# Kernel optimization log

Hardware: AMD Instinct MI355X
Metric: run time of the kernel (lower is better)

The kernel has to match this reference:

```python
import jax, jax.numpy as jnp
import numpy as np

B, H, K, T, OUT, NH = 512, 512, 6, 60, 2, 8

def _gelu(x):
    return jax.nn.gelu(x, approximate=False)  # torch nn.GELU default = exact erf

def _layernorm(x, g, b, eps=1e-5):
    m = jnp.mean(x, axis=-1, keepdims=True)
    v = jnp.var(x, axis=-1, keepdims=True)
    return (x - m) * jax.lax.rsqrt(v + eps) * g + b

def setup_inputs() -> dict:
    key = jax.random.key(0)
    ks = iter(jax.random.split(key, 40))
    def p(shape, scale=0.02):
        return jax.random.normal(next(ks), shape, dtype=jnp.float32) * scale
    return dict(
        interaction_ctx=p((B, H), 1.0),
        cooperative_ctx=p((B, H), 1.0),
        map_ctx=p((B, H), 1.0),
        mode_queries=p((K, H)),
        # context_proj: Linear(3H,H) -> GELU -> Linear(H,H)
        Wc1=p((3 * H, H)), bc1=jnp.zeros((H,), jnp.float32),
        Wc2=p((H, H)), bc2=jnp.zeros((H,), jnp.float32),
        # coarse_heads stacked over modes: Linear(H,2H)->GELU->Linear(2H,T*OUT)
        Wk1=p((K, H, 2 * H)), bk1=jnp.zeros((K, 2 * H), jnp.float32),
        Wk2=p((K, 2 * H, T * OUT)), bk2=jnp.zeros((K, T * OUT), jnp.float32),
        # traj_encoder: Linear(OUT,H)->GELU
        Wt=p((OUT, H)), bt=jnp.zeros((H,), jnp.float32),
        # refine_attn (MultiheadAttention) projections
        Wq_a=p((H, H)), bq_a=jnp.zeros((H,), jnp.float32),
        Wk_a=p((H, H)), bk_a=jnp.zeros((H,), jnp.float32),
        Wv_a=p((H, H)), bv_a=jnp.zeros((H,), jnp.float32),
        Wo_a=p((H, H)), bo_a=jnp.zeros((H,), jnp.float32),
        ln_g=jnp.ones((H,), jnp.float32), ln_b=jnp.zeros((H,), jnp.float32),
        # refine_heads stacked over modes: Linear(H,H)->GELU->Linear(H,OUT)
        Wr1=p((K, H, H)), br1=jnp.zeros((K, H), jnp.float32),
        Wr2=p((K, H, OUT)), br2=jnp.zeros((K, OUT), jnp.float32),
        # conf_head: Linear(H,64)->ReLU->Linear(64,1)
        Wf1=p((H, 64)), bf1=jnp.zeros((64,), jnp.float32),
        Wf2=p((64, 1)), bf2=jnp.zeros((1,), jnp.float32),
    )

def reference(interaction_ctx, cooperative_ctx, map_ctx, mode_queries,
              Wc1, bc1, Wc2, bc2, Wk1, bk1, Wk2, bk2, Wt, bt,
              Wq_a, bq_a, Wk_a, bk_a, Wv_a, bv_a, Wo_a, bo_a,
              ln_g, ln_b, Wr1, br1, Wr2, br2, Wf1, bf1, Wf2, bf2):
    # dropout layers are identity in eval mode
    combined = jnp.concatenate([interaction_ctx, cooperative_ctx, map_ctx], axis=-1)  # (B,3H)
    context = _gelu(combined @ Wc1 + bc1) @ Wc2 + bc2                                 # (B,H)
    mode_features = mode_queries[None, :, :] + context[:, None, :]                    # (B,K,H)

    # coarse heads: per-mode loop -> grouped GEMM over mode axis
    h = _gelu(jnp.einsum('bkh,khf->bkf', mode_features, Wk1) + bk1)                   # (B,K,2H)
    coarse = (jnp.einsum('bkf,kfo->bko', h, Wk2) + bk2).reshape(B, K, T, OUT)          # (B,K,T,OUT)

    traj_feats = _gelu(coarse @ Wt + bt)                                              # (B,K,T,H)

    # refine_attn: keys/values are context broadcast over T (all identical), so
    # softmax weights are exactly uniform and attention output == out_proj(v_ctx).
    # (grads through Wq_a/Wk_a are exactly zero for the same reason.)
    v = context @ Wv_a + bv_a                                                         # (B,H)
    attn_out = v @ Wo_a + bo_a                                                        # (B,H)

    refined_feats = _layernorm(traj_feats + attn_out[:, None, None, :], ln_g, ln_b)   # (B,K,T,H)

    # refine heads: grouped GEMM over mode axis
    r = _gelu(jnp.einsum('bkth,khf->bktf', refined_feats, Wr1) + br1[:, None, :])     # (B,K,T,H)
    offsets = jnp.einsum('bktf,kfo->bkto', r, Wr2) + br2[:, None, :]                  # (B,K,T,OUT)
    predictions = coarse + offsets

    conf = jax.nn.relu(mode_features @ Wf1 + bf1) @ Wf2 + bf2                         # (B,K,1)
    mode_probs = jax.nn.softmax(conf[..., 0], axis=-1)                                # (B,K)
    return predictions, mode_probs
```

## Files before the change

kernel.cpp:

```cpp
#include <hip/hip_runtime.h>
#include <math.h>

#define BB 512
#define HH 512
#define KK 6
#define TT 60
#define OO 2
#define H2 1024
#define TO 120
#define RFP 520
#define HSP 1032

typedef __bf16 bf16x8 __attribute__((ext_vector_type(8)));
typedef float  f32x4  __attribute__((ext_vector_type(4)));
typedef float  f32x16 __attribute__((ext_vector_type(16)));

__device__ __forceinline__ float bf2f(unsigned short u) {
    union { unsigned int i; float f; } v; v.i = ((unsigned int)u) << 16; return v.f;
}
__device__ __forceinline__ unsigned short f2bf(float f) {
    union { float f; unsigned int i; } v; v.f = f;
    unsigned int b = v.i;
    return (unsigned short)((b + 0x7FFFu + ((b >> 16) & 1u)) >> 16);
}
__device__ __forceinline__ unsigned int pack2bf(float a, float b) {
    union { __bf16 h[2]; unsigned int u; } v;
    v.h[0] = (__bf16)a; v.h[1] = (__bf16)b;
    return v.u;
}
__device__ __forceinline__ float gelu_exact(float x) {
    return 0.5f * x * (1.0f + erff(x * 0.70710678118654752f));
}

#if defined(__has_builtin)
#  if __has_builtin(__builtin_amdgcn_rcpf)
#    define FAST_RCP(x) __builtin_amdgcn_rcpf(x)
#  endif
#  if __has_builtin(__builtin_amdgcn_exp2f)
#    define FAST_EXP2(x) __builtin_amdgcn_exp2f(x)
#  endif
#endif
#ifndef FAST_RCP
#  define FAST_RCP(x) (1.0f / (x))
#endif
#ifndef FAST_EXP2
#  define FAST_EXP2(x) __expf((x) * 0.69314718056f)
#endif

__device__ __forceinline__ float gelu_cheap(float x) {
    float x2 = x * x;
    float z = x * fmaf(0.10294324f, x2, 2.3022082f);
    float e = FAST_EXP2(-z);
    return x * FAST_RCP(1.0f + e);
}

struct F8 { float v[8]; };
__device__ __forceinline__ F8 load8f(const float* p) {
    F8 r;
    float4 a = *(const float4*)p;
    float4 b = *(const float4*)(p + 4);
    r.v[0] = a.x; r.v[1] = a.y; r.v[2] = a.z; r.v[3] = a.w;
    r.v[4] = b.x; r.v[5] = b.y; r.v[6] = b.z; r.v[7] = b.w;
    return r;
}
__device__ __forceinline__ F8 load8b(const unsigned short* p) {
    ushort4 a = *(const ushort4*)p;
    ushort4 b = *(const ushort4*)(p + 4);
    F8 r;
    r.v[0] = bf2f(a.x); r.v[1] = bf2f(a.y); r.v[2] = bf2f(a.z); r.v[3] = bf2f(a.w);
    r.v[4] = bf2f(b.x); r.v[5] = bf2f(b.y); r.v[6] = bf2f(b.z); r.v[7] = bf2f(b.w);
    return r;
}

struct PKD { const float* src; unsigned short* dst; int F, N, NC, nch, steps, Z; };
struct PK8 { PKD e[8]; };

__global__ void k_pack(PK8 d) {
    int rid = blockIdx.x * 4 + (threadIdx.x >> 6);
    const int ln = threadIdx.x & 63;
    int i = 0;
    while (i < 7) {
        int tot = d.e[i].Z * d.e[i].nch * d.e[i].steps;
        if (rid < tot) break;
        rid -= tot; ++i;
    }
    const PKD e = d.e[i];
    const int per = e.nch * e.steps;
    const int z = rid / per;
    const int r = rid - z * per;
    const int nch = r / e.steps, step = r - nch * e.steps;
    const float* src = e.src + (size_t)z * e.F * e.N;
    unsigned short* dst = e.dst + ((size_t)z * per + r) * 512 + ln * 8;
    int f_base, n;
    if (e.NC == 16) { f_base = step * 32 + (ln >> 4) * 8; n = nch * 16 + (ln & 15); }
    else            { f_base = step * 16 + (ln >> 5) * 8; n = nch * 32 + (ln & 31); }
    if (n >= e.N) n = e.N - 1;
    unsigned int pk[4];
#pragma unroll
    for (int j = 0; j < 4; ++j) {
        unsigned short lo = f2bf(src[(size_t)(f_base + 2 * j) * e.N + n]);
        unsigned short hi = f2bf(src[(size_t)(f_base + 2 * j + 1) * e.N + n]);
        pk[j] = (unsigned int)lo | ((unsigned int)hi << 16);
    }
    *(uint4*)dst = make_uint4(pk[0], pk[1], pk[2], pk[3]);
}

template <bool CONCAT, bool GELU>
__launch_bounds__(256)
__global__ void k_gemm_m(const void* __restrict__ A0, const void* __restrict__ A1,
                         const void* __restrict__ A2, const unsigned short* __restrict__ BP,
                         const float* __restrict__ bias, unsigned short* __restrict__ C,
                         int Kd) {
    __shared__ __align__(16) unsigned short As[32 * RFP];
    const int tid = threadIdx.x;
    const int bm = blockIdx.x * 32;
    const int bn = blockIdx.y * 32;
    const int w = tid >> 6, ln = tid & 63;
    const int lane15 = ln & 15, quad = ln >> 4;
    const int mh = w >> 1;
    const int ng = w & 1;
    const int n = bn + ng * 16 + lane15;
    const int nchunks = Kd / HH;
    const int stepsTot = Kd / 32;
    const int nchB = blockIdx.y * 2 + ng;

    f32x4 acc0 = {0.f, 0.f, 0.f, 0.f};

    for (int kc = 0; kc < nchunks; ++kc) {
        {
            int r = tid >> 3, c0 = (tid & 7) * 64;
            unsigned short* dp = As + r * RFP + c0;
            if (CONCAT) {
                const float* src = (kc == 0) ? (const float*)A0
                                 : (kc == 1) ? (const float*)A1 : (const float*)A2;
                const float* sp = src + (bm + r) * HH + c0;
                for (int c = 0; c < 64; c += 8) {
                    F8 v = load8f(sp + c);
                    unsigned int pk[4];
#pragma unroll
                    for (int j = 0; j < 4; ++j)
                        pk[j] = pack2bf(v.v[2 * j], v.v[2 * j + 1]);
                    *(uint4*)(dp + c) = make_uint4(pk[0], pk[1], pk[2], pk[3]);
                }
            } else {
                const unsigned short* sp = (const unsigned short*)A0 + (bm + r) * HH + c0;
                for (int c = 0; c < 64; c += 8)
                    *(uint4*)(dp + c) = *(const uint4*)(sp + c);
            }
        }
        __syncthreads();
        const unsigned short* bp = BP + ((size_t)nchB * stepsTot + kc * 16) * 512 + ln * 8;
#pragma unroll
        for (int f0 = 0; f0 < HH; f0 += 32) {
            bf16x8 a0 = *(const bf16x8*)(As + (mh * 16 + lane15) * RFP + f0 + quad * 8);
            bf16x8 bf = *(const bf16x8*)(bp);
            bp += 512;
            acc0 = __builtin_amdgcn_mfma_f32_16x16x32_bf16(a0, bf, acc0, 0, 0, 0);
        }
        __syncthreads();
    }
    const float bb = bias[n];
#pragma unroll
    for (int reg = 0; reg < 4; ++reg) {
        float v0 = acc0[reg] + bb;
        if (GELU) v0 = gelu_exact(v0);
        C[(bm + mh * 16 + quad * 4 + reg) * HH + n] = f2bf(v0);
    }
}

__launch_bounds__(512)
__global__ void k_bcg(const unsigned short* __restrict__ ctx, const float* __restrict__ mq,
                      const unsigned short* __restrict__ Wk1P, const float* __restrict__ bk1,
                      const unsigned short* __restrict__ Wk2P, const float* __restrict__ bk2,
                      const unsigned short* __restrict__ Wf1P, const float* __restrict__ bf1,
                      const float* __restrict__ Wf2, const float* __restrict__ bf2v,
                      unsigned short* __restrict__ coarse_out, float* __restrict__ conf_out,
                      const unsigned short* __restrict__ WvP, const float* __restrict__ bv,
                      unsigned short* __restrict__ vout)
{
    __shared__ __align__(16) unsigned short shbuf[24832];

    const int tid = threadIdx.x;
    const int w = tid >> 6;
    const int ln = tid & 63;
    const int lane15 = ln & 15;
    const int quad = ln >> 4;

    if (blockIdx.x >= 192) {
        unsigned short* As = shbuf;
        const int gbid = blockIdx.x - 192;
        const int bm = (gbid & 15) * 32;
        const int gy = gbid >> 4;
        const int bn = gy * 64;
        const int mh = w >> 2;
        const int ng = w & 3;
        const int n = bn + ng * 16 + lane15;
        const int nchB = gy * 4 + ng;

        {
            int r = tid >> 4, c0 = (tid & 15) * 32;
            const unsigned short* sp = ctx + (bm + r) * HH + c0;
            unsigned short* dp = As + r * RFP + c0;
            for (int c = 0; c < 32; c += 8)
                *(uint4*)(dp + c) = *(const uint4*)(sp + c);
        }
        __syncthreads();
        f32x4 acc0 = {0.f, 0.f, 0.f, 0.f};
        const unsigned short* bp = WvP + (size_t)nchB * 16 * 512 + ln * 8;
#pragma unroll
        for (int f0 = 0; f0 < HH; f0 += 32) {
            bf16x8 a0 = *(const bf16x8*)(As + (mh * 16 + lane15) * RFP + f0 + quad * 8);
            bf16x8 bf = *(const bf16x8*)(bp);
            bp += 512;
            acc0 = __builtin_amdgcn_mfma_f32_16x16x32_bf16(a0, bf, acc0, 0, 0, 0);
        }
        const float bb = bv[n];
#pragma unroll
        for (int reg = 0; reg < 4; ++reg)
            vout[(bm + mh * 16 + quad * 4 + reg) * HH + n] = f2bf(acc0[reg] + bb);
        return;
    }

    unsigned short* mf = shbuf;
    unsigned short* hs = shbuf + 16 * RFP;
    const int k = blockIdx.x % KK;
    const int b0 = (blockIdx.x / KK) * 16;

    {
        int r = tid >> 5;
        int c0 = (tid & 31) * 16;
        const unsigned short* cp = ctx + (b0 + r) * HH + c0;
        const float* qp = mq + k * HH + c0;
        unsigned short* dp = mf + r * RFP + c0;
        for (int c = 0; c < 16; c += 8) {
            F8 cv = load8b(cp + c);
            F8 qv = load8f(qp + c);
            unsigned int pk[4];
#pragma unroll
            for (int j = 0; j < 4; ++j)
                pk[j] = pack2bf(cv.v[2 * j] + qv.v[2 * j], cv.v[2 * j + 1] + qv.v[2 * j + 1]);
            *(uint4*)(dp + c) = make_uint4(pk[0], pk[1], pk[2], pk[3]);
        }
    }
    __syncthreads();

    {
        const unsigned short* wk1p = Wk1P + (size_t)k * (64 * 16 * 512);
        const float* bk1p = bk1 + k * H2;
        for (int g = 0; g < 8; ++g) {
            const int n = w * 128 + g * 16 + lane15;
            f32x4 acc0 = {0.f,0.f,0.f,0.f};
            const unsigned short* bp = wk1p + (size_t)((w * 8 + g) * 16) * 512 + ln * 8;
#pragma unroll
            for (int f0 = 0; f0 < HH; f0 += 32) {
                bf16x8 a0 = *(const bf16x8*)(mf + lane15 * RFP + f0 + quad * 8);
                bf16x8 bf = *(const bf16x8*)(bp);
                bp += 512;
                acc0 = __builtin_amdgcn_mfma_f32_16x16x32_bf16(a0, bf, acc0, 0, 0, 0);
            }
            const float bias = bk1p[n];
#pragma unroll
            for (int reg = 0; reg < 4; ++reg)
                hs[(quad * 4 + reg) * HSP + n] = f2bf(gelu_exact(acc0[reg] + bias));
        }
    }
    __syncthreads();

    {
        const unsigned short* wk2p = Wk2P + (size_t)k * (8 * 32 * 512);
        const int n = w * 16 + lane15;
        f32x4 acc0 = {0.f,0.f,0.f,0.f};
        const unsigned short* bp = wk2p + (size_t)(w * 32) * 512 + ln * 8;
#pragma unroll
        for (int f0 = 0; f0 < H2; f0 += 32) {
            bf16x8 a0 = *(const bf16x8*)(hs + lane15 * HSP + f0 + quad * 8);
            bf16x8 bf = *(const bf16x8*)(bp);
            bp += 512;
            acc0 = __builtin_amdgcn_mfma_f32_16x16x32_bf16(a0, bf, acc0, 0, 0, 0);
        }
        if (n < TO) {
            const float bias = bk2[k * TO + n];
#pragma unroll
            for (int reg = 0; reg < 4; ++reg)
                coarse_out[((b0 + quad * 4 + reg) * KK + k) * TO + n] = f2bf(acc0[reg] + bias);
        }
    }

    if (w == 0) {
        f32x4 acc[4];
#pragma unroll
        for (int nt = 0; nt < 4; ++nt) { f32x4 z = {0.f,0.f,0.f,0.f}; acc[nt] = z; }
#pragma unroll
        for (int f0 = 0; f0 < HH; f0 += 32) {
            const int step = f0 >> 5;
            bf16x8 a0 = *(const bf16x8*)(mf + lane15 * RFP + f0 + quad * 8);
#pragma unroll
            for (int nt = 0; nt < 4; ++nt) {
                bf16x8 bf = *(const bf16x8*)(Wf1P + (size_t)(nt * 16 + step) * 512 + ln * 8);
                acc[nt] = __builtin_amdgcn_mfma_f32_16x16x32_bf16(a0, bf, acc[nt], 0, 0, 0);
            }
        }
        const float b2 = bf2v[0];
#pragma unroll
        for (int reg = 0; reg < 4; ++reg) {
            float s = 0.f;
#pragma unroll
            for (int nt = 0; nt < 4; ++nt) {
                const int n = nt * 16 + lane15;
                s = fmaf(fmaxf(acc[nt][reg] + bf1[n], 0.f), Wf2[n], s);
            }
#pragma unroll
            for (int off = 1; off < 16; off <<= 1) s += __shfl_xor(s, off);
            if (lane15 == 0)
                conf_out[(b0 + quad * 4 + reg) * KK + k] = s + b2;
        }
    }
}

__launch_bounds__(512, 4)
__global__ void k_ef(
    const unsigned short* __restrict__ attn, const unsigned short* __restrict__ coarse_ws,
    const float* __restrict__ Wt,  const float* __restrict__ bt,
    const float* __restrict__ lng, const float* __restrict__ lnb,
    const unsigned short* __restrict__ Wr1P, const float* __restrict__ br1,
    const float* __restrict__ Wr2, const float* __restrict__ br2,
    float* __restrict__ pred_out,
    const float* __restrict__ conf, float* __restrict__ probs)
{
    __shared__ __align__(16) unsigned short rf[64 * RFP];
    __shared__ float coarse[TO];
    __shared__ float br1s[HH];
    __shared__ float2 wr2s[HH];
    __shared__ float po2[8][64][2];

    const int tid = threadIdx.x;
    const int b = blockIdx.x / KK;
    const int k = blockIdx.x % KK;
    const int w = tid >> 6;
    const int ln = tid & 63;
    const int lane31 = ln & 31;
    const int hf = ln >> 5;
    const int cbase = ln * 8;

    const unsigned short* attb = attn + b * HH;

    if (tid < TO) coarse[tid] = bf2f(coarse_ws[(b * KK + k) * TO + tid]);
    br1s[tid] = br1[k * HH + tid];
    wr2s[tid] = ((const float2*)Wr2)[(size_t)k * HH + tid];

    if (k == 0 && tid == 448) {
        float v[KK]; float m = -1e30f;
#pragma unroll
        for (int i = 0; i < KK; ++i) { v[i] = conf[b * KK + i]; m = fmaxf(m, v[i]); }
        float s = 0.f;
#pragma unroll
        for (int i = 0; i < KK; ++i) { v[i] = __expf(v[i] - m); s += v[i]; }
        float inv = 1.0f / s;
#pragma unroll
        for (int i = 0; i < KK; ++i) probs[b * KK + i] = v[i] * inv;
    }
    __syncthreads();

    {
        F8 w0 = load8f(Wt + cbase);
        F8 w1 = load8f(Wt + HH + cbase);
        F8 b8 = load8f(bt + cbase);
        F8 g8 = load8f(lng + cbase);
        F8 bb8 = load8f(lnb + cbase);
        F8 a8 = load8b(attb + cbase);
#pragma unroll
        for (int g = 0; g < 2; ++g) {
            float x[4][8];
            float s[4], s2[4];
#pragma unroll
            for (int r = 0; r < 4; ++r) {
                const int t = w + 8 * (g * 4 + r);
                float ss = 0.f, ss2 = 0.f;
                if (t < 60) {
                    const float co0 = coarse[2 * t], co1 = coarse[2 * t + 1];
#pragma unroll
                    for (int j = 0; j < 8; ++j) {
                        float vv = fmaf(co0, w0.v[j], fmaf(co1, w1.v[j], b8.v[j]));
                        vv = gelu_cheap(vv) + a8.v[j];
                        x[r][j] = vv; ss += vv; ss2 = fmaf(vv, vv, ss2);
                    }
                } else {
#pragma unroll
                    for (int j = 0; j < 8; ++j) x[r][j] = 0.f;
                }
                s[r] = ss; s2[r] = ss2;
            }
#pragma unroll
            for (int off = 32; off > 0; off >>= 1) {
#pragma unroll
                for (int r = 0; r < 4; ++r) {
                    s[r] += __shfl_xor(s[r], off);
                    s2[r] += __shfl_xor(s2[r], off);
                }
            }
#pragma unroll
            for (int r = 0; r < 4; ++r) {
                const int t = w + 8 * (g * 4 + r);
                if (t < 60) {
                    float mean = s[r] * (1.0f / HH);
                    float var = fmaf(-mean, mean, s2[r] * (1.0f / HH));
                    float inv = rsqrtf(var + 1e-5f);
                    unsigned int pk[4];
#pragma unroll
                    for (int j = 0; j < 4; ++j) {
                        float y0 = fmaf((x[r][2 * j] - mean) * inv, g8.v[2 * j], bb8.v[2 * j]);
                        float y1 = fmaf((x[r][2 * j + 1] - mean) * inv, g8.v[2 * j + 1], bb8.v[2 * j + 1]);
                        pk[j] = pack2bf(y0, y1);
                    }
                    *(uint4*)(rf + t * RFP + cbase) = make_uint4(pk[0], pk[1], pk[2], pk[3]);
                } else {
                    *(uint4*)(rf + t * RFP + cbase) = make_uint4(0, 0, 0, 0);
                }
            }
        }
    }
    __syncthreads();

    {
        const unsigned short* bp0 = Wr1P + (size_t)k * (16 * 32 * 512)
                                  + (size_t)(w * 2) * 32 * 512 + ln * 8;
        const unsigned short* bp1 = bp0 + 32 * 512;
        const int n0 = w * 64;
        const unsigned short* a0p = rf + lane31 * RFP + hf * 8;
        const unsigned short* a1p = a0p + 32 * RFP;

        f32x16 acc00 = {0.f,0.f,0.f,0.f,0.f,0.f,0.f,0.f,0.f,0.f,0.f,0.f,0.f,0.f,0.f,0.f};
        f32x16 acc01 = acc00, acc10 = acc00, acc11 = acc00;

        __builtin_amdgcn_s_setprio(1);
#pragma unroll
        for (int st = 0; st < 32; ++st) {
            const int k0 = st * 16;
            bf16x8 A0 = *(const bf16x8*)(a0p + k0);
            bf16x8 A1 = *(const bf16x8*)(a1p + k0);
            bf16x8 B0 = *(const bf16x8*)(bp0 + st * 512);
            bf16x8 B1 = *(const bf16x8*)(bp1 + st * 512);
            acc00 = __builtin_amdgcn_mfma_f32_32x32x16_bf16(B0, A0, acc00, 0, 0, 0);
            acc01 = __builtin_amdgcn_mfma_f32_32x32x16_bf16(B1, A0, acc01, 0, 0, 0);
            acc10 = __builtin_amdgcn_mfma_f32_32x32x16_bf16(B0, A1, acc10, 0, 0, 0);
            acc11 = __builtin_amdgcn_mfma_f32_32x32x16_bf16(B1, A1, acc11, 0, 0, 0);
        }
        __builtin_amdgcn_s_setprio(0);

        float p00 = 0.f, p01 = 0.f, p10 = 0.f, p11 = 0.f;
#pragma unroll
        for (int nt = 0; nt < 2; ++nt) {
#pragma unroll
            for (int reg = 0; reg < 16; ++reg) {
                const int n = n0 + nt * 32 + (reg & 3) + 8 * (reg >> 2) + 4 * hf;
                const float bb = br1s[n];
                const float2 w2 = wr2s[n];
                const float a0v = nt ? acc01[reg] : acc00[reg];
                const float a1v = nt ? acc11[reg] : acc10[reg];
                const float rv0 = gelu_cheap(a0v + bb);
                const float rv1 = gelu_cheap(a1v + bb);
                p00 = fmaf(rv0, w2.x, p00);
                p01 = fmaf(rv0, w2.y, p01);
                p10 = fmaf(rv1, w2.x, p10);
                p11 = fmaf(rv1, w2.y, p11);
            }
        }
        p00 += __shfl_xor(p00, 32);
        p01 += __shfl_xor(p01, 32);
        p10 += __shfl_xor(p10, 32);
        p11 += __shfl_xor(p11, 32);
        if (ln < 32) {
            *(float2*)&po2[w][lane31][0]      = make_float2(p00, p01);
            *(float2*)&po2[w][32 + lane31][0] = make_float2(p10, p11);
        }
    }
    __syncthreads();

    if (tid < TO) {
        int t = tid >> 1, o = tid & 1;
        float s = 0.f;
#pragma unroll
        for (int ww = 0; ww < 8; ++ww) s += po2[ww][t][o];
        pred_out[((b * KK + k) * TT + t) * 2 + o] = coarse[tid] + s + br2[k * 2 + o];
    }
}

extern "C" void kernel_launch(void* const* d_in, const int* in_sizes, int n_in,
                              void* d_out, int out_size, void* d_ws, size_t ws_size,
                              hipStream_t stream) {
    const float* I0  = (const float*)d_in[0];
    const float* I1  = (const float*)d_in[1];
    const float* I2  = (const float*)d_in[2];
    const float* MQ  = (const float*)d_in[3];
    const float* Wc1 = (const float*)d_in[4];
    const float* bc1 = (const float*)d_in[5];
    const float* Wc2 = (const float*)d_in[6];
    const float* bc2 = (const float*)d_in[7];
    const float* Wk1 = (const float*)d_in[8];
    const float* bk1 = (const float*)d_in[9];
    const float* Wk2 = (const float*)d_in[10];
    const float* bk2 = (const float*)d_in[11];
    const float* Wt  = (const float*)d_in[12];
    const float* bt  = (const float*)d_in[13];
    const float* Wv  = (const float*)d_in[18];
    const float* bv  = (const float*)d_in[19];
    const float* Wo  = (const float*)d_in[20];
    const float* bo  = (const float*)d_in[21];
    const float* lng = (const float*)d_in[22];
    const float* lnb = (const float*)d_in[23];
    const float* Wr1 = (const float*)d_in[24];
    const float* br1 = (const float*)d_in[25];
    const float* Wr2 = (const float*)d_in[26];
    const float* br2 = (const float*)d_in[27];
    const float* Wf1 = (const float*)d_in[28];
    const float* bf1 = (const float*)d_in[29];
    const float* Wf2 = (const float*)d_in[30];
    const float* bf2v = (const float*)d_in[31];

    unsigned short* wsu   = (unsigned short*)d_ws;
    unsigned short* wc1p  = wsu;
    unsigned short* wc2p  = wsu + 786432;
    unsigned short* wvp   = wsu + 1048576;
    unsigned short* wop   = wsu + 1310720;
    unsigned short* wk1p  = wsu + 1572864;
    unsigned short* wk2p  = wsu + 4718592;
    unsigned short* wf1p  = wsu + 5505024;
    unsigned short* wr1p  = wsu + 5537792;
    unsigned short* ctx   = wsu + 7110656;
    unsigned short* attn  = wsu + 7372800;
    unsigned short* tmp   = wsu + 7634944;
    unsigned short* coarse= wsu + 7897088;
    float* conf = (float*)(wsu + 8265728);

    float* pred = (float*)d_out;
    float* probs = pred + BB * KK * TT * OO;

    PK8 pk;
    pk.e[0] = {Wc1, wc1p, 3 * HH, HH, 16, 32, 48, 1};
    pk.e[1] = {Wc2, wc2p, HH, HH, 16, 32, 16, 1};
    pk.e[2] = {Wv,  wvp,  HH, HH, 16, 32, 16, 1};
    pk.e[3] = {Wo,  wop,  HH, HH, 16, 32, 16, 1};
    pk.e[4] = {Wk1, wk1p, HH, H2, 16, 64, 16, KK};
    pk.e[5] = {Wk2, wk2p, H2, TO, 16, 8, 32, KK};
    pk.e[6] = {Wf1, wf1p, HH, 64, 16, 4, 16, 1};
    pk.e[7] = {Wr1, wr1p, HH, HH, 32, 16, 32, KK};
    k_pack<<<dim3(3472), 256, 0, stream>>>(pk);

    k_gemm_m<true,  true ><<<dim3(16, 16), 256, 0, stream>>>(I0, I1, I2, wc1p, bc1, tmp, 3 * HH);
    k_gemm_m<false, false><<<dim3(16, 16), 256, 0, stream>>>(tmp, nullptr, nullptr, wc2p, bc2, ctx, HH);

    k_bcg<<<dim3(320), 512, 0, stream>>>(ctx, MQ, wk1p, bk1, wk2p, bk2, wf1p, bf1, Wf2, bf2v,
                                         coarse, conf, wvp, bv, tmp);

    k_gemm_m<false, false><<<dim3(16, 16), 256, 0, stream>>>(tmp, nullptr, nullptr, wop, bo, attn, HH);

    k_ef<<<dim3(BB * KK), 512, 0, stream>>>(attn, coarse, Wt, bt, lng, lnb,
                                            wr1p, br1, Wr2, br2, pred, conf, probs);
}
```

Measured before the change: 313.8 us.

## Fold Wv and Wo into one product matrix, computed alongside the first context GEMM

Since attn_out = (ctx·Wv + bv)·Wo + bo is linear, the change precomputes Wvo = Wv·Wo and bvo = bv·Wo + bo inside a new kernel that also runs the first context-projection GEMM. The bcg kernel then produces attn directly with a single GEMM, which removes the separate Wo GEMM launch and the intermediate v buffer. The Wv packing step is dropped (its pack entry now repeats Wc2 with zero column chunks). The cost is a weight-weight GEMM on every call plus a serial 512-length dot product per output column for the bias. Rounding changes because the fused weight is stored in bf16.

```diff
diff --git a/kernel.cpp b/kernel.cpp
--- a/kernel.cpp
+++ b/kernel.cpp
@@ -168,6 +168,108 @@
     }
 }
 
+__launch_bounds__(256)
+__global__ void k_g1w(const float* __restrict__ I0, const float* __restrict__ I1,
+                      const float* __restrict__ I2, const unsigned short* __restrict__ Wc1P,
+                      const float* __restrict__ bc1, unsigned short* __restrict__ tmp,
+                      const float* __restrict__ Wv, const unsigned short* __restrict__ WoP,
+                      const float* __restrict__ WoF, const float* __restrict__ bv,
+                      const float* __restrict__ bo,
+                      unsigned short* __restrict__ wvop, float* __restrict__ bvo)
+{
+    __shared__ __align__(16) unsigned short As[32 * RFP];
+    const int tid = threadIdx.x;
+    const int w = tid >> 6, ln = tid & 63;
+    const int lane15 = ln & 15, quad = ln >> 4;
+    const int mh = w >> 1, ng = w & 1;
+
+    if (blockIdx.x >= 256) {
+        const int gbid = blockIdx.x - 256;
+        const int bm = (gbid & 15) * 32;
+        const int bn = (gbid >> 4) * 32;
+        {
+            int r = tid >> 3, c0 = (tid & 7) * 64;
+            const float* sp = Wv + (size_t)(bm + r) * HH + c0;
+            unsigned short* dp = As + r * RFP + c0;
+            for (int c = 0; c < 64; c += 8) {
+                F8 v = load8f(sp + c);
+                unsigned int pk[4];
+#pragma unroll
+                for (int j = 0; j < 4; ++j)
+                    pk[j] = pack2bf(v.v[2 * j], v.v[2 * j + 1]);
+                *(uint4*)(dp + c) = make_uint4(pk[0], pk[1], pk[2], pk[3]);
+            }
+        }
+        __syncthreads();
+        const int n = bn + ng * 16 + lane15;
+        const int nchB = (bn >> 4) + ng;
+        f32x4 acc0 = {0.f, 0.f, 0.f, 0.f};
+        const unsigned short* bp = WoP + (size_t)nchB * 16 * 512 + ln * 8;
+#pragma unroll
+        for (int f0 = 0; f0 < HH; f0 += 32) {
+            bf16x8 a0 = *(const bf16x8*)(As + (mh * 16 + lane15) * RFP + f0 + quad * 8);
+            bf16x8 bf = *(const bf16x8*)(bp);
+            bp += 512;
+            acc0 = __builtin_amdgcn_mfma_f32_16x16x32_bf16(a0, bf, acc0, 0, 0, 0);
+        }
+        const int step2 = bm >> 5;
+        const int nch2 = n >> 4;
+#pragma unroll
+        for (int reg = 0; reg < 4; ++reg) {
+            const int r5 = mh * 16 + quad * 4 + reg;
+            const int ln2 = ((r5 >> 3) << 4) | lane15;
+            wvop[((size_t)(nch2 * 16 + step2)) * 512 + ln2 * 8 + (r5 & 7)] = f2bf(acc0[reg]);
+        }
+        if (bm == 0 && w == 0 && ln < 32) {
+            const int nn = bn + ln;
+            float s = 0.f;
+            for (int f = 0; f < HH; ++f) s = fmaf(bv[f], WoF[(size_t)f * HH + nn], s);
+            bvo[nn] = s + bo[nn];
+        }
+        return;
+    }
+
+    const int bm = (blockIdx.x & 15) * 32;
+    const int by = blockIdx.x >> 4;
+    const int bn = by * 32;
+    const int n = bn + ng * 16 + lane15;
+    const int nchB = by * 2 + ng;
+    const int stepsTot = 48;
+
+    f32x4 acc0 = {0.f, 0.f, 0.f, 0.f};
+
+    for (int kc = 0; kc < 3; ++kc) {
+        {
+            int r = tid >> 3, c0 = (tid & 7) * 64;
+            unsigned short* dp = As + r * RFP + c0;
+            const float* src = (kc == 0) ? I0 : (kc == 1) ? I1 : I2;
+            const float* sp = src + (size_t)(bm + r) * HH + c0;
+            for (int c = 0; c < 64; c += 8) {
+                F8 v = load8f(sp + c);
+                unsigned int pk[4];
+#pragma unroll
+                for (int j = 0; j < 4; ++j)
+                    pk[j] = pack2bf(v.v[2 * j], v.v[2 * j + 1]);
+                *(uint4*)(dp + c) = make_uint4(pk[0], pk[1], pk[2], pk[3]);
+            }
+        }
+        __syncthreads();
+        const unsigned short* bp = Wc1P + ((size_t)nchB * stepsTot + kc * 16) * 512 + ln * 8;
+#pragma unroll
+        for (int f0 = 0; f0 < HH; f0 += 32) {
+            bf16x8 a0 = *(const bf16x8*)(As + (mh * 16 + lane15) * RFP + f0 + quad * 8);
+            bf16x8 bf = *(const bf16x8*)(bp);
+            bp += 512;
+            acc0 = __builtin_amdgcn_mfma_f32_16x16x32_bf16(a0, bf, acc0, 0, 0, 0);
+        }
+        __syncthreads();
+    }
+    const float bb = bc1[n];
+#pragma unroll
+    for (int reg = 0; reg < 4; ++reg)
+        tmp[(bm + mh * 16 + quad * 4 + reg) * HH + n] = f2bf(gelu_exact(acc0[reg] + bb));
+}
+
 __launch_bounds__(512)
 __global__ void k_bcg(const unsigned short* __restrict__ ctx, const float* __restrict__ mq,
                       const unsigned short* __restrict__ Wk1P, const float* __restrict__ bk1,
@@ -175,8 +277,8 @@
                       const unsigned short* __restrict__ Wf1P, const float* __restrict__ bf1,
                       const float* __restrict__ Wf2, const float* __restrict__ bf2v,
                       unsigned short* __restrict__ coarse_out, float* __restrict__ conf_out,
-                      const unsigned short* __restrict__ WvP, const float* __restrict__ bv,
-                      unsigned short* __restrict__ vout)
+                      const unsigned short* __restrict__ WvoP, const float* __restrict__ bvo,
+                      unsigned short* __restrict__ attn_out)
 {
     __shared__ __align__(16) unsigned short shbuf[24832];
 
@@ -206,7 +308,7 @@
         }
         __syncthreads();
         f32x4 acc0 = {0.f, 0.f, 0.f, 0.f};
-        const unsigned short* bp = WvP + (size_t)nchB * 16 * 512 + ln * 8;
+        const unsigned short* bp = WvoP + (size_t)nchB * 16 * 512 + ln * 8;
 #pragma unroll
         for (int f0 = 0; f0 < HH; f0 += 32) {
             bf16x8 a0 = *(const bf16x8*)(As + (mh * 16 + lane15) * RFP + f0 + quad * 8);
@@ -214,10 +316,10 @@
             bp += 512;
             acc0 = __builtin_amdgcn_mfma_f32_16x16x32_bf16(a0, bf, acc0, 0, 0, 0);
         }
-        const float bb = bv[n];
+        const float bb = bvo[n];
 #pragma unroll
         for (int reg = 0; reg < 4; ++reg)
-            vout[(bm + mh * 16 + quad * 4 + reg) * HH + n] = f2bf(acc0[reg] + bb);
+            attn_out[(bm + mh * 16 + quad * 4 + reg) * HH + n] = f2bf(acc0[reg] + bb);
         return;
     }
 
@@ -520,7 +622,7 @@
     unsigned short* wsu   = (unsigned short*)d_ws;
     unsigned short* wc1p  = wsu;
     unsigned short* wc2p  = wsu + 786432;
-    unsigned short* wvp   = wsu + 1048576;
+    unsigned short* wvop  = wsu + 1048576;
     unsigned short* wop   = wsu + 1310720;
     unsigned short* wk1p  = wsu + 1572864;
     unsigned short* wk2p  = wsu + 4718592;
@@ -531,6 +633,7 @@
     unsigned short* tmp   = wsu + 7634944;
     unsigned short* coarse= wsu + 7897088;
     float* conf = (float*)(wsu + 8265728);
+    float* bvo  = (float*)(wsu + 8271872);
 
     float* pred = (float*)d_out;
     float* probs = pred + BB * KK * TT * OO;
@@ -538,21 +641,21 @@
     PK8 pk;
     pk.e[0] = {Wc1, wc1p, 3 * HH, HH, 16, 32, 48, 1};
     pk.e[1] = {Wc2, wc2p, HH, HH, 16, 32, 16, 1};
-    pk.e[2] = {Wv,  wvp,  HH, HH, 16, 32, 16, 1};
+    pk.e[2] = {Wc2, wc2p, HH, HH, 16, 0, 16, 1};
     pk.e[3] = {Wo,  wop,  HH, HH, 16, 32, 16, 1};
     pk.e[4] = {Wk1, wk1p, HH, H2, 16, 64, 16, KK};
     pk.e[5] = {Wk2, wk2p, H2, TO, 16, 8, 32, KK};
     pk.e[6] = {Wf1, wf1p, HH, 64, 16, 4, 16, 1};
     pk.e[7] = {Wr1, wr1p, HH, HH, 32, 16, 32, KK};
-    k_pack<<<dim3(3472), 256, 0, stream>>>(pk);
-
-    k_gemm_m<true,  true ><<<dim3(16, 16), 256, 0, stream>>>(I0, I1, I2, wc1p, bc1, tmp, 3 * HH);
+    k_pack<<<dim3(3344), 256, 0, stream>>>(pk);
+
+    k_g1w<<<dim3(512), 256, 0, stream>>>(I0, I1, I2, wc1p, bc1, tmp,
+                                         Wv, wop, Wo, bv, bo, wvop, bvo);
+
     k_gemm_m<false, false><<<dim3(16, 16), 256, 0, stream>>>(tmp, nullptr, nullptr, wc2p, bc2, ctx, HH);
 
     k_bcg<<<dim3(320), 512, 0, stream>>>(ctx, MQ, wk1p, bk1, wk2p, bk2, wf1p, bf1, Wf2, bf2v,
-                                         coarse, conf, wvp, bv, tmp);
-
-    k_gemm_m<false, false><<<dim3(16, 16), 256, 0, stream>>>(tmp, nullptr, nullptr, wop, bo, attn, HH);
+                                         coarse, conf, wvop, bvo, attn);
 
     k_ef<<<dim3(BB * KK), 512, 0, stream>>>(attn, coarse, Wt, bt, lng, lnb,
                                             wr1p, br1, Wr2, br2, pred, conf, probs);
```

Result: slower. 322.4 us (+2.7%).
